# Performance work log

Hardware: AMD Instinct MI355X
Metric: run time of the kernel (lower is better)

The kernel has to match this reference:

```python
import jax, jax.numpy as jnp
import numpy as np

B, D, C, H = 65536, 256, 128, 1024
SPLIT = D // 2           # transformed half (odd indices under 'even' mask)
NET_IN = (D - SPLIT) + C # unchanged half + cond


def setup_inputs() -> dict:
    key = jax.random.key(0)
    ks = jax.random.split(key, 10)
    s = 0.02
    return {
        "x": jax.random.normal(ks[0], (B, D), jnp.float32),
        "cond": jax.random.normal(ks[1], (B, C), jnp.float32),
        "W1": jax.random.normal(ks[2], (NET_IN, H), jnp.float32) * s,
        "b1": jnp.zeros((H,), jnp.float32),
        "W2": jax.random.normal(ks[3], (H, H), jnp.float32) * s,
        "b2": jnp.zeros((H,), jnp.float32),
        "Ws": jax.random.normal(ks[4], (H, SPLIT), jnp.float32) * s,
        "bs": jnp.zeros((SPLIT,), jnp.float32),
        "Wt": jax.random.normal(ks[5], (H, SPLIT), jnp.float32) * s,
        "bt": jnp.zeros((SPLIT,), jnp.float32),
    }


def reference(x, cond, W1, b1, W2, b2, Ws, bs, Wt, bt):
    d = x.shape[1]
    even = jnp.arange(0, d, 2)  # mask==1 -> unchanged (x1)
    odd = jnp.arange(1, d, 2)   # mask==0 -> transformed (x2)
    x1u = x[:, even]            # (B, d - d//2)
    x2u = x[:, odd]             # (B, d//2)
    h = jax.nn.relu(jnp.concatenate([x1u, cond], axis=1) @ W1 + b1)
    h = jax.nn.relu(h @ W2 + b2)
    log_s = jnp.tanh(h @ Ws + bs)
    t = h @ Wt + bt
    x2t = x2u * jnp.exp(log_s) + t
    out = jnp.zeros_like(x).at[:, even].set(x1u).at[:, odd].set(x2t)
    log_det = jnp.sum(log_s, axis=1)
    return out, log_det
```

## Files before the change

kernel.cpp:

```cpp
#include <hip/hip_runtime.h>
#include <hip/hip_bf16.h>
#include <math.h>

#define B_ROWS 65536
#define D_DIM 256
#define C_DIM 128
#define H_DIM 1024

typedef __bf16 bf16x8 __attribute__((ext_vector_type(8)));
typedef float f32x4 __attribute__((ext_vector_type(4)));
typedef short short8 __attribute__((ext_vector_type(8)));

__device__ __forceinline__ unsigned short f2bf(float f) {
    unsigned int u = __float_as_uint(f);
    u += 0x7fffu + ((u >> 16) & 1u);
    return (unsigned short)(u >> 16);
}

__device__ __forceinline__ void gl2lds16(const void* g, void* l) {
    __builtin_amdgcn_global_load_lds(
        (const __attribute__((address_space(1))) unsigned int*)g,
        (__attribute__((address_space(3))) unsigned int*)l, 16, 0, 0);
}

__device__ __forceinline__ bf16x8 ds_read_b128_asm(const short* p) {
    bf16x8 r;
    asm volatile("ds_read_b128 %0, %1"
                 : "=v"(r)
                 : "v"((const __attribute__((address_space(3))) short*)p));
    return r;
}

__device__ __forceinline__ void swizzle_mn(int id, int mtiles, int& m, int& n) {
    if ((mtiles & 7) == 0) {
        int g = id >> 6, r = id & 63;
        m = g * 8 + (r & 7);
        n = r >> 3;
    } else {
        m = id >> 3;
        n = id & 7;
    }
}

__global__ void transpose_bf16(const float* __restrict__ src, short* __restrict__ dst,
                               int R, int C, int total) {
    int tid = blockIdx.x * 256 + threadIdx.x;
    if (tid >= total) return;
    int per = R >> 3;
    int n = tid / per;
    int k0 = (tid - n * per) << 3;
    short8 o;
#pragma unroll
    for (int j = 0; j < 8; ++j) o[j] = (short)f2bf(src[(size_t)(k0 + j) * C + n]);
    *(short8*)&dst[(size_t)n * R + k0] = o;
}

__global__ void prep_b3(const float* __restrict__ bs, const float* __restrict__ bt,
                        float* __restrict__ b3) {
    int i = threadIdx.x;
    b3[i] = (i < 128) ? bs[i] : bt[i - 128];
}

__global__ __launch_bounds__(256) void prep_a(
    const float* __restrict__ x, const float* __restrict__ cond,
    short* __restrict__ A) {
    int t = blockIdx.x * 256 + threadIdx.x;
    int m = t >> 5, seg = t & 31;
    short8 o;
    if (seg < 16) {
        const float4* p = (const float4*)(x + (size_t)m * 256 + seg * 16);
        float4 a = p[0], b = p[1], c = p[2], d = p[3];
        o[0] = (short)f2bf(a.x); o[1] = (short)f2bf(a.z);
        o[2] = (short)f2bf(b.x); o[3] = (short)f2bf(b.z);
        o[4] = (short)f2bf(c.x); o[5] = (short)f2bf(c.z);
        o[6] = (short)f2bf(d.x); o[7] = (short)f2bf(d.z);
    } else {
        const float4* p = (const float4*)(cond + (size_t)m * 128 + (seg - 16) * 8);
        float4 a = p[0], b = p[1];
        o[0] = (short)f2bf(a.x); o[1] = (short)f2bf(a.y);
        o[2] = (short)f2bf(a.z); o[3] = (short)f2bf(a.w);
        o[4] = (short)f2bf(b.x); o[5] = (short)f2bf(b.y);
        o[6] = (short)f2bf(b.z); o[7] = (short)f2bf(b.w);
    }
    *(short8*)&A[(size_t)m * 256 + seg * 8] = o;
}

__global__ __launch_bounds__(256) void gemm_tn(
    const short* __restrict__ A, const short* __restrict__ Bw,
    const float* __restrict__ bias, unsigned short* __restrict__ Cout,
    int mtiles, int N, int K) {
    constexpr int BK = 64;
    __shared__ __align__(16) short As[128 * BK];
    __shared__ __align__(16) short Bs[128 * BK];
    const int tid = threadIdx.x;
    const int lane = tid & 63;
    const int wave = tid >> 6;
    int mt, nt;
    swizzle_mn(blockIdx.x, mtiles, mt, nt);
    const int tm = mt * 128, tn = nt * 128;
    const int mo = (wave >> 1) * 64;
    const int no = (wave & 1) * 64;

    f32x4 acc[4][4];
#pragma unroll
    for (int i = 0; i < 4; ++i)
#pragma unroll
        for (int j = 0; j < 4; ++j) acc[i][j] = f32x4{0.f, 0.f, 0.f, 0.f};

    const int srow = lane >> 3;
    const int skb = (lane & 7) ^ srow;

    for (int kc = 0; kc < K; kc += BK) {
        __syncthreads();
#pragma unroll
        for (int i = 0; i < 4; ++i) {
            int c = wave * 4 + i;
            int row = c * 8 + srow;
            gl2lds16(A + (size_t)(tm + row) * K + kc + skb * 8, &As[c * 512]);
            gl2lds16(Bw + (size_t)(tn + row) * K + kc + skb * 8, &Bs[c * 512]);
        }
        __syncthreads();
#pragma unroll
        for (int kk = 0; kk < 2; ++kk) {
            bf16x8 af[4], bfr[4];
            int kb = kk * 4 + (lane >> 4);
#pragma unroll
            for (int t = 0; t < 4; ++t) {
                int r = mo + t * 16 + (lane & 15);
                af[t] = *(const bf16x8*)&As[r * BK + ((kb ^ (r & 7)) << 3)];
                int n = no + t * 16 + (lane & 15);
                bfr[t] = *(const bf16x8*)&Bs[n * BK + ((kb ^ (n & 7)) << 3)];
            }
#pragma unroll
            for (int i = 0; i < 4; ++i)
#pragma unroll
                for (int j = 0; j < 4; ++j)
                    acc[i][j] = __builtin_amdgcn_mfma_f32_16x16x32_bf16(
                        af[i], bfr[j], acc[i][j], 0, 0, 0);
        }
    }

#pragma unroll
    for (int j = 0; j < 4; ++j) {
        int col = tn + no + j * 16 + (lane & 15);
        float bb = bias[col];
#pragma unroll
        for (int i = 0; i < 4; ++i) {
            int row0 = tm + mo + i * 16 + ((lane >> 4) << 2);
            f32x4 v = acc[i][j];
#pragma unroll
            for (int rr = 0; rr < 4; ++rr)
                Cout[(size_t)(row0 + rr) * N + col] = f2bf(fmaxf(v[rr] + bb, 0.f));
        }
    }
}

template<int K>
__global__ __launch_bounds__(512, 2) void gemm2_8ph(
    const short* __restrict__ A, const short* __restrict__ Bw,
    const float* __restrict__ bias, unsigned short* __restrict__ Cout) {
    constexpr int NT = K / 64;
    constexpr unsigned OFF_A0 = 0, OFF_B0 = 16384, OFF_A1 = 32768, OFF_B1 = 49152;
    __shared__ __align__(16) short smem[65536];

    const int tid = threadIdx.x;
    const int lane = tid & 63;
    const int wave = tid >> 6;
    const int wm = wave >> 2;
    const int wn = wave & 3;
    const int l15 = lane & 15;
    const int quad = lane >> 4;
    const int srow = lane >> 3;
    const int skb8 = ((lane & 7) ^ srow) << 3;

    const int id = blockIdx.x, nwg = gridDim.x;
    const int xcd = id & 7, lid = id >> 3;
    const int q = nwg >> 3, r = nwg & 7;
    const int wgid = (xcd < r ? xcd * (q + 1) : r * (q + 1) + (xcd - r) * q) + lid;
    const int mt = wgid >> 2, nt = wgid & 3;
    const size_t Abase = (size_t)(mt * 256) * K;
    const size_t Bbase = (size_t)(nt * 256) * K;

    f32x4 acc[8][4];
#pragma unroll
    for (int m = 0; m < 8; ++m)
#pragma unroll
        for (int n = 0; n < 4; ++n) acc[m][n] = f32x4{0.f, 0.f, 0.f, 0.f};

    bf16x8 af[2][2] = {};
    bf16x8 bfr[4][2] = {};

    auto stage2 = [&](unsigned off, const short* g, size_t rowbase, int kc, int c0, int c1) {
        gl2lds16(g + rowbase + (size_t)(c0 * 8 + srow) * K + kc + skb8, smem + off + c0 * 512);
        gl2lds16(g + rowbase + (size_t)(c1 * 8 + srow) * K + kc + skb8, smem + off + c1 * 512);
    };
    auto stageU = [&](int u, unsigned aOff, unsigned bOff, int kc) {
        if (u == 0)      stage2(bOff, Bw, Bbase, kc, wave * 2, wave * 2 + 1);
        else if (u == 1) stage2(bOff, Bw, Bbase, kc, 16 + wave * 2, 17 + wave * 2);
        else if (u == 2) stage2(aOff, A, Abase, kc, wave, 16 + wave);
        else             stage2(aOff, A, Abase, kc, 8 + wave, 24 + wave);
    };

    const unsigned x0 = (unsigned)((quad ^ (l15 & 7)) << 3);
    const unsigned x1 = (unsigned)(((4 + quad) ^ (l15 & 7)) << 3);

    auto mfma8 = [&](int pprev) {
        __builtin_amdgcn_s_setprio(1);
#pragma unroll
        for (int kk = 0; kk < 2; ++kk)
#pragma unroll
            for (int mm = 0; mm < 2; ++mm)
#pragma unroll
                for (int n = 0; n < 4; ++n)
                    acc[pprev * 2 + mm][n] = __builtin_amdgcn_mfma_f32_16x16x32_bf16(
                        af[mm][kk], bfr[n][kk], acc[pprev * 2 + mm][n], 0, 0, 0);
        __builtin_amdgcn_s_setprio(0);
    };

    auto slot = [&](int ph, int w, unsigned caOff, unsigned cbOff,
                    unsigned naOff, unsigned nbOff) {
        if (ph & 1) {
            if (w < NT - 2) asm volatile("s_waitcnt vmcnt(6)" ::: "memory");
            else            asm volatile("s_waitcnt vmcnt(0)" ::: "memory");
        }
        __builtin_amdgcn_sched_barrier(0);
        __builtin_amdgcn_s_barrier();
        __builtin_amdgcn_sched_barrier(0);
        if (ph == 0) { if (w + 1 < NT) stageU(3, naOff, nbOff, (w + 1) << 6); }
        else         { if (w + 2 < NT) stageU(ph - 1, caOff, cbOff, (w + 2) << 6); }
        __builtin_amdgcn_sched_barrier(0);
        asm volatile("s_waitcnt lgkmcnt(0)" ::: "memory");
        __builtin_amdgcn_sched_barrier(0);
        mfma8((ph + 3) & 3);
        __builtin_amdgcn_sched_barrier(0);
        const short* aA = smem + caOff + ((wm << 7) + l15) * 64;
        const short* aB = smem + cbOff + ((wn << 6) + l15) * 64;
        if (ph == 0) {
#pragma unroll
            for (int n = 0; n < 4; ++n) {
                bfr[n][0] = ds_read_b128_asm(aB + n * 1024 + x0);
                bfr[n][1] = ds_read_b128_asm(aB + n * 1024 + x1);
            }
        }
#pragma unroll
        for (int mm = 0; mm < 2; ++mm) {
            af[mm][0] = ds_read_b128_asm(aA + (ph * 2 + mm) * 1024 + x0);
            af[mm][1] = ds_read_b128_asm(aA + (ph * 2 + mm) * 1024 + x1);
        }
        __builtin_amdgcn_sched_barrier(0);
    };

    stageU(0, OFF_A0, OFF_B0, 0);
    stageU(1, OFF_A0, OFF_B0, 0);
    stageU(2, OFF_A0, OFF_B0, 0);
    stageU(3, OFF_A0, OFF_B0, 0);
    stageU(0, OFF_A1, OFF_B1, 64);
    stageU(1, OFF_A1, OFF_B1, 64);
    stageU(2, OFF_A1, OFF_B1, 64);
    asm volatile("s_waitcnt vmcnt(6)" ::: "memory");

#pragma unroll 1
    for (int w = 0; w < NT; w += 2) {
#pragma unroll
        for (int ph = 0; ph < 4; ++ph)
            slot(ph, w, OFF_A0, OFF_B0, OFF_A1, OFF_B1);
#pragma unroll
        for (int ph = 0; ph < 4; ++ph)
            slot(ph, w + 1, OFF_A1, OFF_B1, OFF_A0, OFF_B0);
    }
    asm volatile("s_waitcnt lgkmcnt(0)" ::: "memory");
    __builtin_amdgcn_sched_barrier(0);
    mfma8(3);

    __syncthreads();
    unsigned short* cs = (unsigned short*)smem;
#pragma unroll
    for (int n = 0; n < 4; ++n) {
        int colblk = wn * 4 + n;
        int col = (colblk << 4) + l15;
        float bb = bias[nt * 256 + col];
#pragma unroll
        for (int m = 0; m < 8; ++m) {
            int row = (wm << 7) + m * 16 + (quad << 2);
#pragma unroll
            for (int rr = 0; rr < 4; ++rr) {
                int rw = row + rr;
                int sb = colblk ^ ((rw >> 2) & 3);
                cs[rw * 256 + (sb << 4) + l15] = f2bf(fmaxf(acc[m][n][rr] + bb, 0.f));
            }
        }
    }
    __syncthreads();
    const size_t cbase = (size_t)(mt * 256) * 1024 + nt * 256;
    const int rloc = tid >> 5, cchunk = tid & 31;
#pragma unroll
    for (int rnd = 0; rnd < 16; ++rnd) {
        int rw = rnd * 16 + rloc;
        int blk = cchunk >> 1, half = cchunk & 1;
        int sb = blk ^ ((rw >> 2) & 3);
        short8 v = *(const short8*)&cs[rw * 256 + (sb << 4) + half * 8];
        *(short8*)((unsigned short*)Cout + cbase + (size_t)rw * 1024 + cchunk * 8) = v;
    }
}

__global__ __launch_bounds__(256) void gemm3_final(
    const short* __restrict__ H2, const short* __restrict__ W3T,
    const float* __restrict__ b3, const float* __restrict__ x,
    float* __restrict__ out, float* __restrict__ logdet) {
    constexpr int BK = 64, K = 1024;
    __shared__ __align__(16) char raw[40960];
    __shared__ float rowsum[64];
    short* As = (short*)raw;
    short* Bs = (short*)(raw + 8192);
    float* Tbuf = (float*)raw;
    const int tid = threadIdx.x;
    const int lane = tid & 63;
    const int wave = tid >> 6;
    const int tm = blockIdx.x * 64;
    const int srow = lane >> 3;
    const int skb = (lane & 7) ^ srow;
    const int l15 = lane & 15;
    const int quad = lane >> 4;

    if (tid < 64) rowsum[tid] = 0.f;

    f32x4 acc[4][4];
#pragma unroll
    for (int i = 0; i < 4; ++i)
#pragma unroll
        for (int j = 0; j < 4; ++j) acc[i][j] = f32x4{0.f, 0.f, 0.f, 0.f};

    for (int kc = 0; kc < K; kc += BK) {
        __syncthreads();
#pragma unroll
        for (int i = 0; i < 10; ++i) {
            int c = wave * 10 + i;
            if (c < 8) {
                int row = c * 8 + srow;
                gl2lds16(H2 + (size_t)(tm + row) * K + kc + skb * 8, &As[c * 512]);
            } else {
                int row = (c - 8) * 8 + srow;
                gl2lds16(W3T + (size_t)row * K + kc + skb * 8, &Bs[(c - 8) * 512]);
            }
        }
        __syncthreads();
#pragma unroll
        for (int kk = 0; kk < 2; ++kk) {
            int kb = kk * 4 + quad;
            bf16x8 af[4], bfr[4];
#pragma unroll
            for (int mt = 0; mt < 4; ++mt) {
                int r = mt * 16 + l15;
                af[mt] = *(const bf16x8*)&As[r * BK + ((kb ^ (r & 7)) << 3)];
            }
#pragma unroll
            for (int nt = 0; nt < 4; ++nt) {
                int n = wave * 64 + nt * 16 + l15;
                bfr[nt] = *(const bf16x8*)&Bs[n * BK + ((kb ^ (n & 7)) << 3)];
            }
#pragma unroll
            for (int mt = 0; mt < 4; ++mt)
#pragma unroll
                for (int nt = 0; nt < 4; ++nt)
                    acc[mt][nt] = __builtin_amdgcn_mfma_f32_16x16x32_bf16(
                        af[mt], bfr[nt], acc[mt][nt], 0, 0, 0);
        }
    }

    __syncthreads();
    if (wave >= 2) {
#pragma unroll
        for (int nt = 0; nt < 4; ++nt) {
            int col = wave * 64 + nt * 16 + l15;
            float bb = b3[col];
            int cl = col - 128;
#pragma unroll
            for (int mt = 0; mt < 4; ++mt) {
#pragma unroll
                for (int rr = 0; rr < 4; ++rr) {
                    int m = mt * 16 + quad * 4 + rr;
                    Tbuf[m * 132 + cl] = acc[mt][nt][rr] + bb;
                }
            }
        }
    }
    __syncthreads();
    if (wave < 2) {
#pragma unroll
        for (int mt = 0; mt < 4; ++mt) {
#pragma unroll
            for (int rr = 0; rr < 4; ++rr) {
                int m = mt * 16 + quad * 4 + rr;
                int grow = tm + m;
                float s = 0.f;
#pragma unroll
                for (int nt = 0; nt < 4; ++nt) {
                    int j = wave * 64 + nt * 16 + l15;
                    float p = acc[mt][nt][rr] + b3[j];
                    p = fminf(fmaxf(p, -15.f), 15.f);
                    float e2 = __expf(2.f * p);
                    float ls = (e2 - 1.f) / (e2 + 1.f);
                    s += ls;
                    float tt = Tbuf[m * 132 + j];
                    float2 xv = *(const float2*)&x[(size_t)grow * 256 + 2 * j];
                    float2 ov;
                    ov.x = xv.x;
                    ov.y = xv.y * __expf(ls) + tt;
                    *(float2*)&out[(size_t)grow * 256 + 2 * j] = ov;
                }
                s += __shfl_xor(s, 1);
                s += __shfl_xor(s, 2);
                s += __shfl_xor(s, 4);
                s += __shfl_xor(s, 8);
                if (l15 == 0) atomicAdd(&rowsum[m], s);
            }
        }
    }
    __syncthreads();
    if (tid < 64) logdet[tm + tid] = rowsum[tid];
}

extern "C" void kernel_launch(void* const* d_in, const int* in_sizes, int n_in,
                              void* d_out, int out_size, void* d_ws, size_t ws_size,
                              hipStream_t stream) {
    const float* x = (const float*)d_in[0];
    const float* cond = (const float*)d_in[1];
    const float* W1 = (const float*)d_in[2];
    const float* b1 = (const float*)d_in[3];
    const float* W2 = (const float*)d_in[4];
    const float* b2 = (const float*)d_in[5];
    const float* Wsp = (const float*)d_in[6];
    const float* bs = (const float*)d_in[7];
    const float* Wtp = (const float*)d_in[8];
    const float* bt = (const float*)d_in[9];

    char* ws = (char*)d_ws;
    short* W1T = (short*)(ws);
    short* W2T = (short*)(ws + 524288ull);
    short* W3T = (short*)(ws + 2621440ull);
    float* b3  = (float*)(ws + 3145728ull);
    short* Aprep = (short*)(ws + 3149824ull);
    const size_t chunk_base = 3149824ull + 33554432ull;

    int n_chunks = 1;
    while (n_chunks < 512) {
        size_t rp = (size_t)B_ROWS / n_chunks;
        if (chunk_base + rp * 4096ull <= ws_size) break;
        n_chunks *= 2;
    }
    const size_t RP = (size_t)B_ROWS / n_chunks;

    float* out = (float*)d_out;
    float* logdet = out + (size_t)B_ROWS * D_DIM;

    transpose_bf16<<<(32768 + 255) / 256, 256, 0, stream>>>(W1, W1T, 256, 1024, 32768);
    transpose_bf16<<<(131072 + 255) / 256, 256, 0, stream>>>(W2, W2T, 1024, 1024, 131072);
    transpose_bf16<<<(16384 + 255) / 256, 256, 0, stream>>>(Wsp, W3T, 1024, 128, 16384);
    transpose_bf16<<<(16384 + 255) / 256, 256, 0, stream>>>(Wtp, W3T + 131072, 1024, 128, 16384);
    prep_b3<<<1, 256, 0, stream>>>(bs, bt, b3);
    prep_a<<<B_ROWS * 32 / 256, 256, 0, stream>>>(x, cond, Aprep);

    for (int c = 0; c < n_chunks; ++c) {
        const size_t r0 = (size_t)c * RP;
        short* H1 = (short*)(ws + chunk_base);
        short* H2 = (short*)(ws + chunk_base + 2048ull * RP);
        const int mtiles = (int)(RP / 128);

        if ((RP & 255) == 0) {
            gemm2_8ph<256><<<(int)(RP / 256) * 4, 512, 0, stream>>>(
                Aprep + r0 * 256, W1T, b1, (unsigned short*)H1);
            gemm2_8ph<1024><<<(int)(RP / 256) * 4, 512, 0, stream>>>(
                H1, W2T, b2, (unsigned short*)H2);
        } else {
            gemm_tn<<<mtiles * 8, 256, 0, stream>>>(
                Aprep + r0 * 256, W1T, b1, (unsigned short*)H1, mtiles, H_DIM, 256);
            gemm_tn<<<mtiles * 8, 256, 0, stream>>>(
                H1, W2T, b2, (unsigned short*)H2, mtiles, H_DIM, H_DIM);
        }
        gemm3_final<<<(int)(RP / 64), 256, 0, stream>>>(
            H2, W3T, b3, x + r0 * D_DIM, out + r0 * D_DIM, logdet + r0);
    }
}
```

Baseline: 458.6 us.

## Pipeline final GEMM with double-buffered async LDS loads and fuse prep kernels

```diff
diff --git a/kernel.cpp b/kernel.cpp
--- a/kernel.cpp
+++ b/kernel.cpp
@@ -29,6 +29,12 @@
                  : "=v"(r)
                  : "v"((const __attribute__((address_space(3))) short*)p));
     return r;
+}
+
+__device__ __forceinline__ int xcd_swz(int id, int nwg) {
+    int xcd = id & 7, lid = id >> 3;
+    int q = nwg >> 3, r = nwg & 7;
+    return (xcd < r ? xcd * (q + 1) : r * (q + 1) + (xcd - r) * q) + lid;
 }
 
 __device__ __forceinline__ void swizzle_mn(int id, int mtiles, int& m, int& n) {
@@ -42,47 +48,64 @@
     }
 }
 
-__global__ void transpose_bf16(const float* __restrict__ src, short* __restrict__ dst,
-                               int R, int C, int total) {
-    int tid = blockIdx.x * 256 + threadIdx.x;
-    if (tid >= total) return;
-    int per = R >> 3;
-    int n = tid / per;
-    int k0 = (tid - n * per) << 3;
-    short8 o;
-#pragma unroll
-    for (int j = 0; j < 8; ++j) o[j] = (short)f2bf(src[(size_t)(k0 + j) * C + n]);
-    *(short8*)&dst[(size_t)n * R + k0] = o;
-}
-
-__global__ void prep_b3(const float* __restrict__ bs, const float* __restrict__ bt,
-                        float* __restrict__ b3) {
-    int i = threadIdx.x;
-    b3[i] = (i < 128) ? bs[i] : bt[i - 128];
-}
-
-__global__ __launch_bounds__(256) void prep_a(
+__global__ __launch_bounds__(256) void prep_all(
+    const float* __restrict__ W1, const float* __restrict__ W2,
+    const float* __restrict__ Ws, const float* __restrict__ Wt,
+    const float* __restrict__ bs, const float* __restrict__ bt,
     const float* __restrict__ x, const float* __restrict__ cond,
-    short* __restrict__ A) {
+    short* __restrict__ W1T, short* __restrict__ W2T, short* __restrict__ W3T,
+    float* __restrict__ b3, short* __restrict__ A) {
     int t = blockIdx.x * 256 + threadIdx.x;
-    int m = t >> 5, seg = t & 31;
-    short8 o;
-    if (seg < 16) {
-        const float4* p = (const float4*)(x + (size_t)m * 256 + seg * 16);
-        float4 a = p[0], b = p[1], c = p[2], d = p[3];
-        o[0] = (short)f2bf(a.x); o[1] = (short)f2bf(a.z);
-        o[2] = (short)f2bf(b.x); o[3] = (short)f2bf(b.z);
-        o[4] = (short)f2bf(c.x); o[5] = (short)f2bf(c.z);
-        o[6] = (short)f2bf(d.x); o[7] = (short)f2bf(d.z);
+    if (t < 196864) {
+        short8 o;
+        if (t < 32768) {
+            int n = t >> 5, k0 = (t & 31) << 3;
+#pragma unroll
+            for (int j = 0; j < 8; ++j) o[j] = (short)f2bf(W1[(size_t)(k0 + j) * 1024 + n]);
+            *(short8*)&W1T[(size_t)n * 256 + k0] = o;
+        } else if (t < 163840) {
+            int u = t - 32768;
+            int n = u >> 7, k0 = (u & 127) << 3;
+#pragma unroll
+            for (int j = 0; j < 8; ++j) o[j] = (short)f2bf(W2[(size_t)(k0 + j) * 1024 + n]);
+            *(short8*)&W2T[(size_t)n * 1024 + k0] = o;
+        } else if (t < 180224) {
+            int u = t - 163840;
+            int n = u >> 7, k0 = (u & 127) << 3;
+#pragma unroll
+            for (int j = 0; j < 8; ++j) o[j] = (short)f2bf(Ws[(size_t)(k0 + j) * 128 + n]);
+            *(short8*)&W3T[(size_t)n * 1024 + k0] = o;
+        } else if (t < 196608) {
+            int u = t - 180224;
+            int n = u >> 7, k0 = (u & 127) << 3;
+#pragma unroll
+            for (int j = 0; j < 8; ++j) o[j] = (short)f2bf(Wt[(size_t)(k0 + j) * 128 + n]);
+            *(short8*)&W3T[131072 + (size_t)n * 1024 + k0] = o;
+        } else {
+            int i = t - 196608;
+            b3[i] = (i < 128) ? bs[i] : bt[i - 128];
+        }
     } else {
-        const float4* p = (const float4*)(cond + (size_t)m * 128 + (seg - 16) * 8);
-        float4 a = p[0], b = p[1];
-        o[0] = (short)f2bf(a.x); o[1] = (short)f2bf(a.y);
-        o[2] = (short)f2bf(a.z); o[3] = (short)f2bf(a.w);
-        o[4] = (short)f2bf(b.x); o[5] = (short)f2bf(b.y);
-        o[6] = (short)f2bf(b.z); o[7] = (short)f2bf(b.w);
-    }
-    *(short8*)&A[(size_t)m * 256 + seg * 8] = o;
+        int u = t - 196864;
+        int m = u >> 5, seg = u & 31;
+        short8 o;
+        if (seg < 16) {
+            const float4* p = (const float4*)(x + (size_t)m * 256 + seg * 16);
+            float4 a = p[0], b = p[1], c = p[2], d = p[3];
+            o[0] = (short)f2bf(a.x); o[1] = (short)f2bf(a.z);
+            o[2] = (short)f2bf(b.x); o[3] = (short)f2bf(b.z);
+            o[4] = (short)f2bf(c.x); o[5] = (short)f2bf(c.z);
+            o[6] = (short)f2bf(d.x); o[7] = (short)f2bf(d.z);
+        } else {
+            const float4* p = (const float4*)(cond + (size_t)m * 128 + (seg - 16) * 8);
+            float4 a = p[0], b = p[1];
+            o[0] = (short)f2bf(a.x); o[1] = (short)f2bf(a.y);
+            o[2] = (short)f2bf(a.z); o[3] = (short)f2bf(a.w);
+            o[4] = (short)f2bf(b.x); o[5] = (short)f2bf(b.y);
+            o[6] = (short)f2bf(b.z); o[7] = (short)f2bf(b.w);
+        }
+        *(short8*)&A[(size_t)m * 256 + seg * 8] = o;
+    }
 }
 
 __global__ __launch_bounds__(256) void gemm_tn(
@@ -173,10 +196,7 @@
     const int srow = lane >> 3;
     const int skb8 = ((lane & 7) ^ srow) << 3;
 
-    const int id = blockIdx.x, nwg = gridDim.x;
-    const int xcd = id & 7, lid = id >> 3;
-    const int q = nwg >> 3, r = nwg & 7;
-    const int wgid = (xcd < r ? xcd * (q + 1) : r * (q + 1) + (xcd - r) * q) + lid;
+    const int wgid = xcd_swz(blockIdx.x, gridDim.x);
     const int mt = wgid >> 2, nt = wgid & 3;
     const size_t Abase = (size_t)(mt * 256) * K;
     const size_t Bbase = (size_t)(nt * 256) * K;
@@ -303,26 +323,30 @@
     }
 }
 
-__global__ __launch_bounds__(256) void gemm3_final(
+__global__ __launch_bounds__(512, 2) void gemm3_pipe(
     const short* __restrict__ H2, const short* __restrict__ W3T,
     const float* __restrict__ b3, const float* __restrict__ x,
     float* __restrict__ out, float* __restrict__ logdet) {
-    constexpr int BK = 64, K = 1024;
-    __shared__ __align__(16) char raw[40960];
-    __shared__ float rowsum[64];
-    short* As = (short*)raw;
-    short* Bs = (short*)(raw + 8192);
-    float* Tbuf = (float*)raw;
+    constexpr int K = 1024, NT = 16;
+    constexpr unsigned OFF_A0 = 0, OFF_B0 = 8192, OFF_A1 = 24576, OFF_B1 = 32768;
+    __shared__ __align__(16) short smem[49152];
+    __shared__ float rowsum[128];
+
     const int tid = threadIdx.x;
     const int lane = tid & 63;
     const int wave = tid >> 6;
-    const int tm = blockIdx.x * 64;
-    const int srow = lane >> 3;
-    const int skb = (lane & 7) ^ srow;
+    const int wm = wave >> 2;
+    const int wn = wave & 3;
     const int l15 = lane & 15;
     const int quad = lane >> 4;
-
-    if (tid < 64) rowsum[tid] = 0.f;
+    const int srow = lane >> 3;
+    const int skb8 = ((lane & 7) ^ srow) << 3;
+
+    const int mt = xcd_swz(blockIdx.x, gridDim.x);
+    const int tm = mt * 128;
+    const size_t Abase = (size_t)tm * K;
+
+    if (tid < 128) rowsum[tid] = 0.f;
 
     f32x4 acc[4][4];
 #pragma unroll
@@ -330,73 +354,110 @@
 #pragma unroll
         for (int j = 0; j < 4; ++j) acc[i][j] = f32x4{0.f, 0.f, 0.f, 0.f};
 
-    for (int kc = 0; kc < K; kc += BK) {
-        __syncthreads();
-#pragma unroll
-        for (int i = 0; i < 10; ++i) {
-            int c = wave * 10 + i;
-            if (c < 8) {
-                int row = c * 8 + srow;
-                gl2lds16(H2 + (size_t)(tm + row) * K + kc + skb * 8, &As[c * 512]);
-            } else {
-                int row = (c - 8) * 8 + srow;
-                gl2lds16(W3T + (size_t)row * K + kc + skb * 8, &Bs[(c - 8) * 512]);
+    bf16x8 af[2] = {};
+    bf16x8 bfr[4][2] = {};
+
+    auto stage2 = [&](unsigned off, const short* g, size_t rowbase, int kc, int c0, int c1) {
+        gl2lds16(g + rowbase + (size_t)(c0 * 8 + srow) * K + kc + skb8, smem + off + c0 * 512);
+        gl2lds16(g + rowbase + (size_t)(c1 * 8 + srow) * K + kc + skb8, smem + off + c1 * 512);
+    };
+    auto stageA  = [&](unsigned aOff, int kc) { stage2(aOff, H2, Abase, kc, wave, 8 + wave); };
+    auto stageB1 = [&](unsigned bOff, int kc) { stage2(bOff, W3T, 0, kc, 2 * wave, 2 * wave + 1); };
+    auto stageB2 = [&](unsigned bOff, int kc) { stage2(bOff, W3T, 0, kc, 16 + 2 * wave, 17 + 2 * wave); };
+
+    const unsigned x0 = (unsigned)((quad ^ (l15 & 7)) << 3);
+    const unsigned x1 = (unsigned)(((4 + quad) ^ (l15 & 7)) << 3);
+
+    auto mfma4 = [&](int pprev) {
+        __builtin_amdgcn_s_setprio(1);
+#pragma unroll
+        for (int kk = 0; kk < 2; ++kk)
+#pragma unroll
+            for (int n = 0; n < 4; ++n)
+                acc[pprev][n] = __builtin_amdgcn_mfma_f32_16x16x32_bf16(
+                    af[kk], bfr[n][kk], acc[pprev][n], 0, 0, 0);
+        __builtin_amdgcn_s_setprio(0);
+    };
+
+    auto slot = [&](int ph, int w, unsigned caOff, unsigned cbOff, unsigned naOff) {
+        if (w < NT - 2) asm volatile("s_waitcnt vmcnt(4)" ::: "memory");
+        else            asm volatile("s_waitcnt vmcnt(0)" ::: "memory");
+        __builtin_amdgcn_sched_barrier(0);
+        __builtin_amdgcn_s_barrier();
+        __builtin_amdgcn_sched_barrier(0);
+        if (ph == 0)      { if (w + 1 < NT) stageA(naOff, (w + 1) << 6); }
+        else if (ph == 1) { if (w + 2 < NT) stageB1(cbOff, (w + 2) << 6); }
+        else if (ph == 2) { if (w + 2 < NT) stageB2(cbOff, (w + 2) << 6); }
+        __builtin_amdgcn_sched_barrier(0);
+        asm volatile("s_waitcnt lgkmcnt(0)" ::: "memory");
+        __builtin_amdgcn_sched_barrier(0);
+        mfma4((ph + 3) & 3);
+        __builtin_amdgcn_sched_barrier(0);
+        const short* aA = smem + caOff + ((wm << 6) + l15) * 64;
+        const short* aB = smem + cbOff + ((wn << 6) + l15) * 64;
+        if (ph == 0) {
+#pragma unroll
+            for (int n = 0; n < 4; ++n) {
+                bfr[n][0] = ds_read_b128_asm(aB + n * 1024 + x0);
+                bfr[n][1] = ds_read_b128_asm(aB + n * 1024 + x1);
             }
         }
-        __syncthreads();
-#pragma unroll
-        for (int kk = 0; kk < 2; ++kk) {
-            int kb = kk * 4 + quad;
-            bf16x8 af[4], bfr[4];
-#pragma unroll
-            for (int mt = 0; mt < 4; ++mt) {
-                int r = mt * 16 + l15;
-                af[mt] = *(const bf16x8*)&As[r * BK + ((kb ^ (r & 7)) << 3)];
-            }
-#pragma unroll
-            for (int nt = 0; nt < 4; ++nt) {
-                int n = wave * 64 + nt * 16 + l15;
-                bfr[nt] = *(const bf16x8*)&Bs[n * BK + ((kb ^ (n & 7)) << 3)];
-            }
-#pragma unroll
-            for (int mt = 0; mt < 4; ++mt)
-#pragma unroll
-                for (int nt = 0; nt < 4; ++nt)
-                    acc[mt][nt] = __builtin_amdgcn_mfma_f32_16x16x32_bf16(
-                        af[mt], bfr[nt], acc[mt][nt], 0, 0, 0);
-        }
-    }
+        af[0] = ds_read_b128_asm(aA + ph * 1024 + x0);
+        af[1] = ds_read_b128_asm(aA + ph * 1024 + x1);
+        __builtin_amdgcn_sched_barrier(0);
+    };
+
+    stageA(OFF_A0, 0);
+    stageB1(OFF_B0, 0);
+    stageB2(OFF_B0, 0);
+    stageB1(OFF_B1, 64);
+    stageB2(OFF_B1, 64);
+    asm volatile("s_waitcnt vmcnt(4)" ::: "memory");
+
+#pragma unroll 1
+    for (int w = 0; w < NT; w += 2) {
+#pragma unroll
+        for (int ph = 0; ph < 4; ++ph)
+            slot(ph, w, OFF_A0, OFF_B0, OFF_A1);
+#pragma unroll
+        for (int ph = 0; ph < 4; ++ph)
+            slot(ph, w + 1, OFF_A1, OFF_B1, OFF_A0);
+    }
+    asm volatile("s_waitcnt lgkmcnt(0)" ::: "memory");
+    __builtin_amdgcn_sched_barrier(0);
+    mfma4(3);
 
     __syncthreads();
-    if (wave >= 2) {
-#pragma unroll
-        for (int nt = 0; nt < 4; ++nt) {
-            int col = wave * 64 + nt * 16 + l15;
+    float* Tbuf = (float*)smem;
+    if (wn >= 2) {
+#pragma unroll
+        for (int n = 0; n < 4; ++n) {
+            int col = (wn << 6) + n * 16 + l15;
             float bb = b3[col];
             int cl = col - 128;
 #pragma unroll
-            for (int mt = 0; mt < 4; ++mt) {
+            for (int mm = 0; mm < 4; ++mm) {
 #pragma unroll
                 for (int rr = 0; rr < 4; ++rr) {
-                    int m = mt * 16 + quad * 4 + rr;
-                    Tbuf[m * 132 + cl] = acc[mt][nt][rr] + bb;
+                    int m = (wm << 6) + mm * 16 + quad * 4 + rr;
+                    Tbuf[m * 132 + cl] = acc[mm][n][rr] + bb;
                 }
             }
         }
     }
     __syncthreads();
-    if (wave < 2) {
-#pragma unroll
-        for (int mt = 0; mt < 4; ++mt) {
+    if (wn < 2) {
+#pragma unroll
+        for (int mm = 0; mm < 4; ++mm) {
 #pragma unroll
             for (int rr = 0; rr < 4; ++rr) {
-                int m = mt * 16 + quad * 4 + rr;
+                int m = (wm << 6) + mm * 16 + quad * 4 + rr;
                 int grow = tm + m;
                 float s = 0.f;
 #pragma unroll
-                for (int nt = 0; nt < 4; ++nt) {
-                    int j = wave * 64 + nt * 16 + l15;
-                    float p = acc[mt][nt][rr] + b3[j];
+                for (int n = 0; n < 4; ++n) {
+                    int j = (wn << 6) + n * 16 + l15;
+                    float p = acc[mm][n][rr] + b3[j];
                     p = fminf(fmaxf(p, -15.f), 15.f);
                     float e2 = __expf(2.f * p);
                     float ls = (e2 - 1.f) / (e2 + 1.f);
@@ -417,7 +478,7 @@
         }
     }
     __syncthreads();
-    if (tid < 64) logdet[tm + tid] = rowsum[tid];
+    if (tid < 128) logdet[tm + tid] = rowsum[tid];
 }
 
 extern "C" void kernel_launch(void* const* d_in, const int* in_sizes, int n_in,
@@ -453,12 +514,8 @@
     float* out = (float*)d_out;
     float* logdet = out + (size_t)B_ROWS * D_DIM;
 
-    transpose_bf16<<<(32768 + 255) / 256, 256, 0, stream>>>(W1, W1T, 256, 1024, 32768);
-    transpose_bf16<<<(131072 + 255) / 256, 256, 0, stream>>>(W2, W2T, 1024, 1024, 131072);
-    transpose_bf16<<<(16384 + 255) / 256, 256, 0, stream>>>(Wsp, W3T, 1024, 128, 16384);
-    transpose_bf16<<<(16384 + 255) / 256, 256, 0, stream>>>(Wtp, W3T + 131072, 1024, 128, 16384);
-    prep_b3<<<1, 256, 0, stream>>>(bs, bt, b3);
-    prep_a<<<B_ROWS * 32 / 256, 256, 0, stream>>>(x, cond, Aprep);
+    prep_all<<<(196864 + B_ROWS * 32 + 255) / 256, 256, 0, stream>>>(
+        W1, W2, Wsp, Wtp, bs, bt, x, cond, W1T, W2T, W3T, b3, Aprep);
 
     for (int c = 0; c < n_chunks; ++c) {
         const size_t r0 = (size_t)c * RP;
@@ -477,7 +534,7 @@
             gemm_tn<<<mtiles * 8, 256, 0, stream>>>(
                 H1, W2T, b2, (unsigned short*)H2, mtiles, H_DIM, H_DIM);
         }
-        gemm3_final<<<(int)(RP / 64), 256, 0, stream>>>(
+        gemm3_pipe<<<(int)(RP / 128), 512, 0, stream>>>(
             H2, W3T, b3, x + r0 * D_DIM, out + r0 * D_DIM, logdet + r0);
     }
 }
```

Result: faster. 427.3 us (-6.8%).
